# Optimization experiments

Measured on AMD Instinct MI355X. Metric: run time of the kernel, lower is better.

The kernel has to match this reference:

```python
import jax, jax.numpy as jnp
import numpy as np

DIM = 384
DIM_HEAD = 32
HEADS = DIM // DIM_HEAD  # 12
WIN = 8
DIM_FF = 1536
FUSED = DIM + DIM + DIM_FF  # 2304


def setup_inputs() -> dict:
    key = jax.random.key(0)
    ks = jax.random.split(key, 8)
    B, H, W = 16, 64, 64
    x = jax.random.normal(ks[0], (B, DIM, H, W), dtype=jnp.float32)
    s = lambda fan_in: 1.0 / np.sqrt(fan_in)
    w_fused = jax.random.normal(ks[1], (FUSED, DIM), dtype=jnp.float32) * s(DIM)
    w_gate = jax.random.normal(ks[2], (HEADS, DIM), dtype=jnp.float32) * s(DIM)
    b_gate = jnp.full((HEADS,), 0.5, dtype=jnp.float32)  # init_constant_(0.5)
    w_attn_out = jax.random.normal(ks[3], (DIM, DIM), dtype=jnp.float32) * s(DIM)
    w_ff_out = jax.random.normal(ks[4], (DIM, DIM_FF), dtype=jnp.float32) * s(DIM_FF)
    # StarReLU learnable scalars (metaformer defaults)
    sr_scale = jnp.asarray(0.8944, dtype=jnp.float32)
    sr_bias = jnp.asarray(-0.4472, dtype=jnp.float32)
    return {"x": x, "w_fused": w_fused, "w_gate": w_gate, "b_gate": b_gate,
            "w_attn_out": w_attn_out, "w_ff_out": w_ff_out,
            "sr_scale": sr_scale, "sr_bias": sr_bias}


def reference(x, w_fused, w_gate, b_gate, w_attn_out, w_ff_out, sr_scale, sr_bias):
    B, C, H, W = x.shape
    p = WIN
    gh, gw = H // p, W // p
    n = p * p
    # b c (h p1) (w p2) -> (b h w) (p1 p2) c
    xw = x.reshape(B, C, gh, p, gw, p).transpose(0, 2, 4, 3, 5, 1).reshape(B * gh * gw, n, C)
    fused = jnp.einsum('bnc,fc->bnf', xw, w_fused)  # [Bw, n, 2304]
    q, kv, x_ff = jnp.split(fused, [DIM, 2 * DIM], axis=-1)
    # b n (h d) -> b h n d
    q = q.reshape(-1, n, HEADS, DIM_HEAD).transpose(0, 2, 1, 3)
    kv = kv.reshape(-1, n, HEADS, DIM_HEAD).transpose(0, 2, 1, 3)
    scale = 1.0 / np.sqrt(DIM_HEAD)
    scores = jnp.einsum('bhnd,bhmd->bhnm', q, kv) * scale
    attn = jax.nn.softmax(scores, axis=-1)
    x_attn = jnp.einsum('bhnm,bhmd->bhnd', attn, kv)  # kv is both key and value
    gate = jnp.einsum('bnc,hc->bnh', xw, w_gate) + b_gate  # [Bw, n, heads]
    x_attn = x_attn * jax.nn.sigmoid(gate.transpose(0, 2, 1)[..., None])
    x_attn = x_attn.transpose(0, 2, 1, 3).reshape(-1, n, DIM)
    ff = sr_scale * jnp.square(jax.nn.relu(x_ff)) + sr_bias  # StarReLU
    out = jnp.einsum('bnc,oc->bno', x_attn, w_attn_out) + jnp.einsum('bnf,of->bno', ff, w_ff_out)
    # (b h w) (p1 p2) c -> b c (h p1) (w p2)
    out = out.reshape(B, gh, gw, p, p, C).transpose(0, 5, 1, 3, 2, 4).reshape(B, C, H, W)
    return out
```

## Files before the change

kernel.cpp:

```cpp
#include <hip/hip_runtime.h>
#include <hip/hip_bf16.h>

typedef __bf16 bf16x8 __attribute__((ext_vector_type(8), may_alias));
typedef float f32x4 __attribute__((ext_vector_type(4), may_alias));
typedef unsigned short ushort_a __attribute__((may_alias));
typedef unsigned int uint_a __attribute__((may_alias));
typedef unsigned short us8 __attribute__((ext_vector_type(8), may_alias));

#define MFMA(a, b, c) __builtin_amdgcn_mfma_f32_16x16x32_bf16(a, b, c, 0, 0, 0)

__device__ __forceinline__ unsigned short f2bf(float f) {
  return __builtin_bit_cast(unsigned short, (__bf16)f);
}
__device__ __forceinline__ float bf2f(unsigned short u) {
  unsigned v = ((unsigned)u) << 16;
  return __builtin_bit_cast(float, v);
}

__device__ __forceinline__ void kbar() {
  __builtin_amdgcn_sched_barrier(0);
  asm volatile("s_waitcnt lgkmcnt(0)" ::: "memory");
  __builtin_amdgcn_sched_barrier(0);
  __builtin_amdgcn_s_barrier();
  __builtin_amdgcn_sched_barrier(0);
}

#define GLOAD(G, L)                                                          \
  __builtin_amdgcn_global_load_lds(                                          \
      (const __attribute__((address_space(1))) unsigned int*)(G),            \
      (__attribute__((address_space(3))) unsigned int*)(L), 16, 0, 0)

#define OFF_WG 884736
#define OFF_WAO 933888
#define OFF_WFO 1081344
#define OFF_XG 1671168
#define OFF_FUSED 26836992
#define OFF_GATE 177831936

__global__ __launch_bounds__(256) void prep_weights(
    const float* __restrict__ wf, const float* __restrict__ wg,
    const float* __restrict__ wao, const float* __restrict__ wfo,
    unsigned short* __restrict__ ws) {
  int i = blockIdx.x * 256 + threadIdx.x;
  if (i < 884736) { ws[i] = f2bf(wf[i]); return; }
  int j = i - 884736;
  if (j < 49152) { ws[i] = f2bf(j < 4608 ? wg[j] : 0.0f); return; }
  j -= 49152;
  if (j < 147456) { ws[i] = f2bf(wao[j]); return; }
  j -= 147456;
  if (j < 589824) ws[i] = f2bf(wfo[j]);
}

__global__ __launch_bounds__(256) void k0_gather(const float* __restrict__ x,
                                                 unsigned short* __restrict__ xg) {
  __shared__ __align__(16) char As[49152];
  int tid = threadIdx.x, wi = blockIdx.x;
  int b = wi >> 6, ghi = (wi >> 3) & 7, gwi = wi & 7;
  const float* xb = x + (size_t)b * 1572864 + (ghi * 8) * 64 + gwi * 8;
  for (int it = 0; it < 12; ++it) {
    int idx = it * 256 + tid;
    int c = idx % 384, p1 = idx / 384;
    const float* src = xb + (size_t)c * 4096 + p1 * 64;
    float4 v0 = *(const float4*)src, v1 = *(const float4*)(src + 4);
    float f[8] = {v0.x, v0.y, v0.z, v0.w, v1.x, v1.y, v1.z, v1.w};
#pragma unroll
    for (int jj = 0; jj < 8; ++jj) {
      int row = p1 * 8 + jj;
      int byte = (row * 768 + c * 2) ^ ((row & 7) << 4);
      *(ushort_a*)(As + byte) = f2bf(f[jj]);
    }
  }
  __syncthreads();
  unsigned short* og = xg + (size_t)wi * 24576;
#pragma unroll
  for (int it = 0; it < 12; ++it) {
    int idx = it * 256 + tid;
    int row = idx / 48, c = idx % 48;
    int byte = (row * 768 + c * 16) ^ ((row & 7) << 4);
    *(us8*)(og + (size_t)row * 384 + c * 8) = *(us8*)(As + byte);
  }
}

__global__ __launch_bounds__(512, 4) void k1_gemm(unsigned short* __restrict__ ws,
                                                  const float* __restrict__ srs,
                                                  const float* __restrict__ srb) {
  __shared__ __align__(16) char sm[65536];
  const int tid = threadIdx.x, lane = tid & 63, wave = tid >> 6;
  const int l15 = lane & 15, l4 = lane >> 4;
  const int wr = wave & 3, wc = wave >> 2;
  const int bid = blockIdx.x;
  const int swz = (bid & 7) * 1216 + (bid >> 3);
  const int mb = swz / 19, nb = swz - mb * 19;
  const unsigned short* Ab = ws + OFF_XG + (size_t)mb * 128 * 384;
  const unsigned short* Bb =
      (nb < 18) ? ws + (size_t)nb * 128 * 384 : ws + OFF_WG;
  const int srow = tid >> 3, sc = tid & 7;
  f32x4 of[2][4] = {};
  us8 sA0[2], sB0[2], sA1[2], sB1[2];

#define K1_LOAD(KS, SA, SB)                                                   \
  {                                                                           \
    _Pragma("unroll") for (int r2 = 0; r2 < 2; ++r2) {                        \
      int row = srow + 64 * r2;                                               \
      SA[r2] = *(const us8*)(Ab + (size_t)row * 384 + (KS)*64 + sc * 8);      \
      SB[r2] = *(const us8*)(Bb + (size_t)row * 384 + (KS)*64 + sc * 8);      \
    }                                                                         \
  }
#define K1_WRITE(BUF, SA, SB)                                                 \
  {                                                                           \
    _Pragma("unroll") for (int r2 = 0; r2 < 2; ++r2) {                        \
      int row = srow + 64 * r2;                                               \
      int byte = ((row * 128 + sc * 16) ^ ((row & 7) << 4)) + (BUF);          \
      *(us8*)(sm + byte) = SA[r2];                                            \
      *(us8*)(sm + 32768 + byte) = SB[r2];                                    \
    }                                                                         \
  }
#define K1_COMPUTE(BUF)                                                       \
  {                                                                           \
    _Pragma("unroll") for (int kk = 0; kk < 2; ++kk) {                        \
      bf16x8 af[2], bfr[4];                                                   \
      _Pragma("unroll") for (int mt = 0; mt < 2; ++mt) {                      \
        int row = wr * 32 + mt * 16 + l15;                                    \
        af[mt] = *(const bf16x8*)(sm + (BUF) +                                \
                 ((row * 128 + kk * 64 + l4 * 16) ^ ((row & 7) << 4)));       \
      }                                                                       \
      _Pragma("unroll") for (int nt = 0; nt < 4; ++nt) {                      \
        int row = wc * 64 + nt * 16 + l15;                                    \
        bfr[nt] = *(const bf16x8*)(sm + 32768 + (BUF) +                       \
                  ((row * 128 + kk * 64 + l4 * 16) ^ ((row & 7) << 4)));      \
      }                                                                       \
      _Pragma("unroll") for (int mt = 0; mt < 2; ++mt)                        \
      _Pragma("unroll") for (int nt = 0; nt < 4; ++nt)                        \
          of[mt][nt] = MFMA(af[mt], bfr[nt], of[mt][nt]);                     \
    }                                                                         \
  }

  K1_LOAD(0, sA0, sB0);
  K1_LOAD(1, sA1, sB1);
  K1_WRITE(0, sA0, sB0);
  __syncthreads();
#pragma unroll 1
  for (int kp = 0; kp < 3; ++kp) {
    int ks = kp * 2;
    if (ks + 2 < 6) K1_LOAD(ks + 2, sA0, sB0);
    K1_COMPUTE(0);
    K1_WRITE(16384, sA1, sB1);
    kbar();
    if (ks + 3 < 6) K1_LOAD(ks + 3, sA1, sB1);
    K1_COMPUTE(16384);
    if (ks + 2 < 6) K1_WRITE(0, sA0, sB0);
    kbar();
  }
  const float ssc = srs[0], sbi = srb[0];
  const bool ffreg = (nb >= 6) && (nb < 18);
#pragma unroll
  for (int mt = 0; mt < 2; ++mt)
#pragma unroll
    for (int nt = 0; nt < 4; ++nt)
#pragma unroll
      for (int rr = 0; rr < 4; ++rr) {
        int row = wr * 32 + mt * 16 + l4 * 4 + rr;
        int col = wc * 64 + nt * 16 + l15;
        float v = of[mt][nt][rr];
        if (ffreg) { v = fmaxf(v, 0.0f); v = ssc * v * v + sbi; }
        *(ushort_a*)(sm + ((row * 256 + col * 2) ^ ((row & 7) << 4))) = f2bf(v);
      }
  __syncthreads();
  if (nb < 18) {
    unsigned short* fo = ws + OFF_FUSED + (size_t)mb * 128 * 2304 + nb * 128;
#pragma unroll
    for (int r2 = 0; r2 < 4; ++r2) {
      int idx = r2 * 512 + tid;
      int row = idx >> 4, c = idx & 15;
      int byte = (row * 256 + c * 16) ^ ((row & 7) << 4);
      __builtin_nontemporal_store(*(us8*)(sm + byte),
                                  (us8*)(fo + (size_t)row * 2304 + c * 8));
    }
  } else {
    unsigned short* go = ws + OFF_GATE + (size_t)mb * 128 * 16;
#pragma unroll
    for (int r2 = 0; r2 < 4; ++r2) {
      int idx = r2 * 512 + tid;
      int row = idx >> 4, c = idx & 15;
      if (c < 2) {
        int byte = (row * 256 + c * 16) ^ ((row & 7) << 4);
        __builtin_nontemporal_store(*(us8*)(sm + byte),
                                    (us8*)(go + (size_t)row * 16 + c * 8));
      }
    }
  }
}

__global__ __launch_bounds__(256, 3) void k2_attn(unsigned short* __restrict__ ws,
                                                  const float* __restrict__ bgate) {
  __shared__ __align__(16) char sm[49152];
  const int tid = threadIdx.x, lane = tid & 63, wave = tid >> 6;
  const int l15 = lane & 15, l4 = lane >> 4;
  char* kvT = sm + wave * 12288;
  char* Pb = kvT + 4096;
  const int wi = blockIdx.x;
  const size_t T0 = (size_t)wi * 64;
  unsigned short* fused = ws + OFF_FUSED;
  const unsigned short* gb = ws + OFF_GATE;
  const f32x4 zz = {};
#pragma unroll 1
  for (int hi = 0; hi < 3; ++hi) {
    const int h = wave + hi * 4;
    bf16x8 akv[4], bq[4];
#pragma unroll
    for (int t = 0; t < 4; ++t) {
      akv[t] = *(const bf16x8*)(fused + (T0 + t * 16 + l15) * 2304 + 384 + h * 32 + l4 * 8);
      bq[t] = *(const bf16x8*)(fused + (T0 + t * 16 + l15) * 2304 + h * 32 + l4 * 8);
    }
    f32x4 sfT[4][4];
#pragma unroll
    for (int mt = 0; mt < 4; ++mt)
#pragma unroll
      for (int ni = 0; ni < 4; ++ni) sfT[mt][ni] = MFMA(akv[mt], bq[ni], zz);
#pragma unroll
    for (int mt = 0; mt < 4; ++mt) {
      us8 u = __builtin_bit_cast(us8, akv[mt]);
      int m = mt * 16 + l15;
#pragma unroll
      for (int j = 0; j < 8; ++j) {
        int d = l4 * 8 + j;
        *(ushort_a*)(kvT + ((d * 128 + m * 2) ^ ((d & 7) << 4))) = u[j];
      }
    }
#pragma unroll
    for (int ni = 0; ni < 4; ++ni) {
      float s[16];
#pragma unroll
      for (int mt = 0; mt < 4; ++mt)
#pragma unroll
        for (int rr = 0; rr < 4; ++rr)
          s[mt * 4 + rr] = sfT[mt][ni][rr] * 0.176776695f;
      float mx = s[0];
#pragma unroll
      for (int q2 = 1; q2 < 16; ++q2) mx = fmaxf(mx, s[q2]);
      mx = fmaxf(mx, __shfl_xor(mx, 16, 64));
      mx = fmaxf(mx, __shfl_xor(mx, 32, 64));
      float sum = 0.0f;
#pragma unroll
      for (int q2 = 0; q2 < 16; ++q2) {
        s[q2] = __expf(s[q2] - mx);
        sum += s[q2];
      }
      sum += __shfl_xor(sum, 16, 64);
      sum += __shfl_xor(sum, 32, 64);
      float rs = 1.0f / sum;
      int n = ni * 16 + l15;
      int rowb = n * 128, sw = (n & 7) << 4;
#pragma unroll
      for (int mt = 0; mt < 4; ++mt) {
        int m = mt * 16 + l4 * 4;
        unsigned p0 = (unsigned)f2bf(s[mt * 4 + 0] * rs) |
                      ((unsigned)f2bf(s[mt * 4 + 1] * rs) << 16);
        unsigned p1 = (unsigned)f2bf(s[mt * 4 + 2] * rs) |
                      ((unsigned)f2bf(s[mt * 4 + 3] * rs) << 16);
        *(uint_a*)(Pb + ((rowb + m * 2) ^ sw)) = p0;
        *(uint_a*)(Pb + ((rowb + (m + 2) * 2) ^ sw)) = p1;
      }
    }
    f32x4 xo[4][2] = {};
#pragma unroll
    for (int ks = 0; ks < 2; ++ks) {
      bf16x8 bv[2];
#pragma unroll
      for (int dt = 0; dt < 2; ++dt) {
        int d = dt * 16 + l15;
        bv[dt] = *(const bf16x8*)(kvT + ((d * 128 + ks * 64 + l4 * 16) ^ ((d & 7) << 4)));
      }
#pragma unroll
      for (int nt = 0; nt < 4; ++nt) {
        int n = nt * 16 + l15;
        bf16x8 ap = *(const bf16x8*)(Pb + ((n * 128 + ks * 64 + l4 * 16) ^ ((n & 7) << 4)));
        xo[nt][0] = MFMA(ap, bv[0], xo[nt][0]);
        xo[nt][1] = MFMA(ap, bv[1], xo[nt][1]);
      }
    }
    const float bgh = bgate[h];
#pragma unroll
    for (int nt = 0; nt < 4; ++nt)
#pragma unroll
      for (int rr = 0; rr < 4; ++rr) {
        int n = nt * 16 + l4 * 4 + rr;
        float gv = bf2f(gb[(T0 + n) * 16 + h]) + bgh;
        float sg = 1.0f / (1.0f + __expf(-gv));
#pragma unroll
        for (int dt = 0; dt < 2; ++dt)
          fused[(T0 + n) * 2304 + h * 32 + dt * 16 + l15] =
              f2bf(xo[nt][dt][rr] * sg);
      }
  }
}

__global__ __launch_bounds__(256, 3) void k3_gemm(const unsigned short* __restrict__ ws,
                                                  float* __restrict__ out) {
  __shared__ __align__(1024) char sm[32768];
  const int tid = threadIdx.x, lane = tid & 63, wave = tid >> 6;
  const int l15 = lane & 15, l4 = lane >> 4;
  const int wr = wave & 1, wc = wave >> 1;
  const int bid = blockIdx.x;
  const int swz = (bid & 7) * 192 + (bid >> 3);
  const int mb = swz / 3, nB = swz - mb * 3;
  const size_t T0 = (size_t)mb * 128;
  const unsigned short* fA = ws + OFF_FUSED + T0 * 2304;
  const unsigned short* wao = ws + OFF_WAO + (size_t)(nB * 128) * 384;
  const unsigned short* wfo = ws + OFF_WFO + (size_t)(nB * 128) * 1536;
  const int lr = lane >> 3, lc = (lane & 7) ^ lr;
  const int offA = lr * 2304 + lc * 8;
  const int offB384 = lr * 384 + lc * 8;
  const int offB1536 = lr * 1536 + lc * 8;
  f32x4 of[4][4] = {};

#pragma unroll 1
  for (int ks = 0; ks < 30; ++ks) {
    const int ac = ks < 6 ? ks * 64 : 768 + (ks - 6) * 64;
#pragma unroll
    for (int i = 0; i < 4; ++i) {
      const int R = wave * 32 + i * 8;
      GLOAD(fA + (size_t)R * 2304 + ac + offA, sm + R * 128);
      if (ks < 6)
        GLOAD(wao + (size_t)R * 384 + ks * 64 + offB384, sm + 16384 + R * 128);
      else
        GLOAD(wfo + (size_t)R * 1536 + (ks - 6) * 64 + offB1536,
              sm + 16384 + R * 128);
    }
    __syncthreads();
#pragma unroll
    for (int kk = 0; kk < 2; ++kk) {
      bf16x8 af[4], bfr[4];
#pragma unroll
      for (int mt = 0; mt < 4; ++mt) {
        int row = wr * 64 + mt * 16 + l15;
        af[mt] = *(const bf16x8*)(sm +
                 ((row * 128 + kk * 64 + l4 * 16) ^ ((row & 7) << 4)));
      }
#pragma unroll
      for (int nt = 0; nt < 4; ++nt) {
        int row = wc * 64 + nt * 16 + l15;
        bfr[nt] = *(const bf16x8*)(sm + 16384 +
                  ((row * 128 + kk * 64 + l4 * 16) ^ ((row & 7) << 4)));
      }
#pragma unroll
      for (int mt = 0; mt < 4; ++mt)
#pragma unroll
        for (int nt = 0; nt < 4; ++nt)
          of[mt][nt] = MFMA(af[mt], bfr[nt], of[mt][nt]);
    }
    __syncthreads();
  }
#pragma unroll
  for (int mt = 0; mt < 4; ++mt) {
    int n0 = wr * 64 + mt * 16 + l4 * 4;
    int T = (int)T0 + n0;
    int wi = T >> 6, n = T & 63;
    int b = wi >> 6, ghi = (wi >> 3) & 7, gwi = wi & 7;
    float* ob = out + (size_t)b * 1572864 + (size_t)(ghi * 8 + (n >> 3)) * 64 +
                gwi * 8 + (n & 7);
#pragma unroll
    for (int nt = 0; nt < 4; ++nt) {
      int c = nB * 128 + wc * 64 + nt * 16 + l15;
      __builtin_nontemporal_store(of[mt][nt], (f32x4*)(ob + (size_t)c * 4096));
    }
  }
}

extern "C" void kernel_launch(void* const* d_in, const int* in_sizes, int n_in,
                              void* d_out, int out_size, void* d_ws, size_t ws_size,
                              hipStream_t stream) {
  const float* x = (const float*)d_in[0];
  const float* wf = (const float*)d_in[1];
  const float* wg = (const float*)d_in[2];
  const float* bg = (const float*)d_in[3];
  const float* wao = (const float*)d_in[4];
  const float* wfo = (const float*)d_in[5];
  const float* srs = (const float*)d_in[6];
  const float* srb = (const float*)d_in[7];
  unsigned short* ws = (unsigned short*)d_ws;

  prep_weights<<<6528, 256, 0, stream>>>(wf, wg, wao, wfo, ws);
  k0_gather<<<1024, 256, 0, stream>>>(x, ws + OFF_XG);
  k1_gemm<<<512 * 19, 512, 0, stream>>>(ws, srs, srb);
  k2_attn<<<1024, 256, 0, stream>>>(ws, bg);
  k3_gemm<<<512 * 3, 256, 0, stream>>>(ws, (float*)d_out);
}
```

Before: 476.4 us.

## Double-buffer LDS tiles in output GEMM to overlap loads with MFMA

Converts the k3 output GEMM from a single LDS buffer, with a load, sync, compute, sync sequence, to a two-stage ping-pong. The next K-slice is prefetched into the alternate buffer while the current one is consumed, with a vmcnt wait that allows the newer loads to stay in flight. This aims to hide global-load latency behind MFMA work. In exchange LDS per block doubles to 64KB and launch bounds drop from 3 to 2 blocks per CU, which reduces occupancy.

```diff
diff --git a/kernel.cpp b/kernel.cpp
--- a/kernel.cpp
+++ b/kernel.cpp
@@ -295,9 +295,9 @@
   }
 }
 
-__global__ __launch_bounds__(256, 3) void k3_gemm(const unsigned short* __restrict__ ws,
+__global__ __launch_bounds__(256, 2) void k3_gemm(const unsigned short* __restrict__ ws,
                                                   float* __restrict__ out) {
-  __shared__ __align__(1024) char sm[32768];
+  __shared__ __align__(1024) char sm[65536];
   const int tid = threadIdx.x, lane = tid & 63, wave = tid >> 6;
   const int l15 = lane & 15, l4 = lane >> 4;
   const int wr = wave & 1, wc = wave >> 1;
@@ -314,33 +314,47 @@
   const int offB1536 = lr * 1536 + lc * 8;
   f32x4 of[4][4] = {};
 
+#define K3_STAGE(KS, BUF)                                                     \
+  {                                                                           \
+    const int ac_ = (KS) < 6 ? (KS)*64 : 768 + ((KS)-6) * 64;                 \
+    _Pragma("unroll") for (int i = 0; i < 4; ++i) {                           \
+      const int R = wave * 32 + i * 8;                                        \
+      GLOAD(fA + (size_t)R * 2304 + ac_ + offA, sm + (BUF) + R * 128);        \
+      if ((KS) < 6)                                                           \
+        GLOAD(wao + (size_t)R * 384 + (KS)*64 + offB384,                      \
+              sm + 32768 + (BUF) + R * 128);                                  \
+      else                                                                    \
+        GLOAD(wfo + (size_t)R * 1536 + ((KS)-6) * 64 + offB1536,              \
+              sm + 32768 + (BUF) + R * 128);                                  \
+    }                                                                         \
+  }
+
+  K3_STAGE(0, 0);
 #pragma unroll 1
   for (int ks = 0; ks < 30; ++ks) {
-    const int ac = ks < 6 ? ks * 64 : 768 + (ks - 6) * 64;
-#pragma unroll
-    for (int i = 0; i < 4; ++i) {
-      const int R = wave * 32 + i * 8;
-      GLOAD(fA + (size_t)R * 2304 + ac + offA, sm + R * 128);
-      if (ks < 6)
-        GLOAD(wao + (size_t)R * 384 + ks * 64 + offB384, sm + 16384 + R * 128);
-      else
-        GLOAD(wfo + (size_t)R * 1536 + (ks - 6) * 64 + offB1536,
-              sm + 16384 + R * 128);
-    }
-    __syncthreads();
+    const int cur = (ks & 1) * 16384;
+    if (ks + 1 < 30) K3_STAGE(ks + 1, 16384 - cur);
+    __builtin_amdgcn_sched_barrier(0);
+    if (ks + 1 < 30)
+      asm volatile("s_waitcnt vmcnt(8)" ::: "memory");
+    else
+      asm volatile("s_waitcnt vmcnt(0)" ::: "memory");
+    __builtin_amdgcn_sched_barrier(0);
+    __builtin_amdgcn_s_barrier();
+    __builtin_amdgcn_sched_barrier(0);
 #pragma unroll
     for (int kk = 0; kk < 2; ++kk) {
       bf16x8 af[4], bfr[4];
 #pragma unroll
       for (int mt = 0; mt < 4; ++mt) {
         int row = wr * 64 + mt * 16 + l15;
-        af[mt] = *(const bf16x8*)(sm +
+        af[mt] = *(const bf16x8*)(sm + cur +
                  ((row * 128 + kk * 64 + l4 * 16) ^ ((row & 7) << 4)));
       }
 #pragma unroll
       for (int nt = 0; nt < 4; ++nt) {
         int row = wc * 64 + nt * 16 + l15;
-        bfr[nt] = *(const bf16x8*)(sm + 16384 +
+        bfr[nt] = *(const bf16x8*)(sm + 32768 + cur +
                   ((row * 128 + kk * 64 + l4 * 16) ^ ((row & 7) << 4)));
       }
 #pragma unroll
@@ -349,7 +363,7 @@
         for (int nt = 0; nt < 4; ++nt)
           of[mt][nt] = MFMA(af[mt], bfr[nt], of[mt][nt]);
     }
-    __syncthreads();
+    kbar();
   }
 #pragma unroll
   for (int mt = 0; mt < 4; ++mt) {
```

Result: no change. 474.4 us (-0.4%).
